# Performance work log

Measured on AMD Instinct MI355X. Metric: run time of the kernel, lower is better.

The kernel has to match this reference:

```python
import jax, jax.numpy as jnp
import numpy as np

N = 50000      # nodes (B*N flattened)
E = 800000     # edges
IN = 128       # in_channels
HID = 32       # hidden_channels per head
HEADS = 2
OUT = 64       # out_channels
NEG_SLOPE = 0.2


def setup_inputs() -> dict:
    key = jax.random.key(0)
    ks = jax.random.split(key, 10)
    x = jax.random.normal(ks[0], (N, IN), jnp.float32)
    edge_index = jax.random.randint(ks[1], (2, E), 0, N, dtype=jnp.int64)
    s = 0.1
    W1 = jax.random.normal(ks[2], (IN, HEADS * HID), jnp.float32) * s
    a_src1 = jax.random.normal(ks[3], (HEADS, HID), jnp.float32) * s
    a_dst1 = jax.random.normal(ks[4], (HEADS, HID), jnp.float32) * s
    b1 = jnp.zeros((HEADS * HID,), jnp.float32)
    W2 = jax.random.normal(ks[5], (HEADS * HID, OUT), jnp.float32) * s
    a_src2 = jax.random.normal(ks[6], (1, OUT), jnp.float32) * s
    a_dst2 = jax.random.normal(ks[7], (1, OUT), jnp.float32) * s
    b2 = jnp.zeros((OUT,), jnp.float32)
    return {"x": x, "edge_index": edge_index,
            "W1": W1, "a_src1": a_src1, "a_dst1": a_dst1, "b1": b1,
            "W2": W2, "a_src2": a_src2, "a_dst2": a_dst2, "b2": b2}


def gat_conv(x, src, dst, W, a_s, a_d, b, heads, ch, concat):
    """PyG GATConv: per-edge attention, softmax over incoming edges of dst."""
    n = x.shape[0]
    h = (x @ W).reshape(n, heads, ch)                       # [N,H,C]
    al_s = (h * a_s).sum(-1)                                # [N,H]
    al_d = (h * a_d).sum(-1)                                # [N,H]
    e = jax.nn.leaky_relu(al_s[src] + al_d[dst], NEG_SLOPE)  # [E,H]
    e_max = jax.ops.segment_max(e, dst, num_segments=n)     # [N,H]
    ex = jnp.exp(e - e_max[dst])
    denom = jax.ops.segment_sum(ex, dst, num_segments=n)
    coef = ex / (denom[dst] + 1e-16)                         # [E,H]
    out = jax.ops.segment_sum(h[src] * coef[:, :, None], dst, num_segments=n)  # [N,H,C]
    out = out.reshape(n, heads * ch) if concat else out.mean(axis=1)
    return out + b


def reference(x, edge_index, W1, a_src1, a_dst1, b1, W2, a_src2, a_dst2, b2):
    loops = jnp.arange(N, dtype=edge_index.dtype)
    src = jnp.concatenate([edge_index[0], loops])  # add_self_loops=True (PyG default)
    dst = jnp.concatenate([edge_index[1], loops])
    h1 = jax.nn.relu(gat_conv(x, src, dst, W1, a_src1, a_dst1, b1, HEADS, HID, True))
    return gat_conv(h1, src, dst, W2, a_src2, a_dst2, b2, 1, OUT, False)
```

## Files before the change

kernel.cpp:

```cpp
#include <hip/hip_runtime.h>

#define IN_CH   128
#define HIDX    64
#define NEG_SLOPE 0.2f
#define CAP     64
#define BNODES  32
#define NXCD    8
#define SUB     4
#define NSEGT   (NXCD * SUB)
#define SEGCAP  64

static inline size_t align256(size_t x) { return (x + 255) & ~(size_t)255; }

__global__ void k_zero(int* __restrict__ p, int n) {
    int i = blockIdx.x * blockDim.x + threadIdx.x;
    if (i < n) p[i] = 0;
}

__global__ void k_bucket(const int* __restrict__ ei, int E,
                         int* __restrict__ bcnt, unsigned* __restrict__ bkt) {
    int i = blockIdx.x * blockDim.x + threadIdx.x;
    if (i >= E) return;
    unsigned xcd;
    asm volatile("s_getreg_b32 %0, hwreg(HW_REG_XCC_ID)" : "=s"(xcd));
    xcd &= (NXCD - 1);
    const int s = ei[i];
    const int d = ei[E + i];
    const int slot = (d >> 5) * NSEGT + (int)xcd * SUB + (i & (SUB - 1));
    int pos = atomicAdd(&bcnt[slot], 1);
    if (pos < SEGCAP)
        bkt[(size_t)slot * SEGCAP + pos] =
            ((unsigned)(d & (BNODES - 1)) << 16) | (unsigned)s;
}

__global__ __launch_bounds__(256)
void k_fill(const int* __restrict__ bcnt, const unsigned* __restrict__ bkt,
            int N, int* __restrict__ cnt, unsigned short* __restrict__ csrf) {
    __shared__ int lcnt[BNODES];
    const int b = blockIdx.x;
    const int t = threadIdx.x;
    if (t < BNODES) lcnt[t] = 0;
    __syncthreads();
    const int nb = b * BNODES;
    const int w = t >> 6, lane = t & 63;
    for (int seg = w; seg < NSEGT; seg += 4) {
        const int slot = b * NSEGT + seg;
        int m = bcnt[slot]; if (m > SEGCAP) m = SEGCAP;
        const unsigned* sp = bkt + (size_t)slot * SEGCAP;
        for (int i = lane; i < m; i += 64) {
            const unsigned v = sp[i];
            const int dl = v >> 16;
            const int s  = v & 0xFFFF;
            const int r  = atomicAdd(&lcnt[dl], 1);
            if (r < CAP) csrf[(size_t)(nb + dl) * CAP + r] = (unsigned short)s;
        }
    }
    __syncthreads();
    if (t < BNODES && nb + t < N) {
        const int c = lcnt[t];
        cnt[nb + t] = c < CAP ? c : CAP;
    }
}

template <int K, int H, bool RELU_IN>
__global__ __launch_bounds__(256)
void k_gemm(const float* __restrict__ X, const float* __restrict__ W,
            const float* __restrict__ bin,
            const float* __restrict__ a_s, const float* __restrict__ a_d,
            float* __restrict__ Hout, float* __restrict__ als,
            float* __restrict__ ald, int N) {
    constexpr int STR = 68;
    __shared__ float Wl[K * 64];
    __shared__ float xT[K * STR];

    const int t  = threadIdx.x;
    const int nb = blockIdx.x * 64;

    {
        const float4* W4 = (const float4*)W;
        float4* Wl4 = (float4*)Wl;
#pragma unroll
        for (int i = 0; i < (K * 16) / 256; ++i)
            Wl4[i * 256 + t] = W4[i * 256 + t];
    }
    {
        constexpr int QK = K / 4;
        constexpr int RS = 256 / QK;
        const int kq = t % QK;
        const int r0 = t / QK;
        for (int n = r0; n < 64; n += RS) {
            const int node = nb + n;
            const int cn = node < N ? node : N - 1;
            float4 v = *(const float4*)(X + (size_t)cn * K + kq * 4);
            if (RELU_IN) {
                const float4 bv = *(const float4*)(bin + kq * 4);
                v.x = fmaxf(v.x + bv.x, 0.f);
                v.y = fmaxf(v.y + bv.y, 0.f);
                v.z = fmaxf(v.z + bv.z, 0.f);
                v.w = fmaxf(v.w + bv.w, 0.f);
            }
            const int ns = (((n >> 2) ^ (kq & 7)) << 2) + (n & 3);
            xT[(kq * 4 + 0) * STR + ns] = v.x;
            xT[(kq * 4 + 1) * STR + ns] = v.y;
            xT[(kq * 4 + 2) * STR + ns] = v.z;
            xT[(kq * 4 + 3) * STR + ns] = v.w;
        }
    }
    __syncthreads();

    const int cg = t & 15;
    const int ng = t >> 4;

    float acc[4][4] = {{0.f}};
#pragma unroll 4
    for (int k = 0; k < K; ++k) {
        const int xb = ((ng ^ ((k >> 2) & 7)) << 2);
        const float4 xv = *(const float4*)&xT[k * STR + xb];
        const float4 wv = *(const float4*)&Wl[k * 64 + (cg << 2)];
        acc[0][0] += xv.x * wv.x; acc[0][1] += xv.x * wv.y;
        acc[0][2] += xv.x * wv.z; acc[0][3] += xv.x * wv.w;
        acc[1][0] += xv.y * wv.x; acc[1][1] += xv.y * wv.y;
        acc[1][2] += xv.y * wv.z; acc[1][3] += xv.y * wv.w;
        acc[2][0] += xv.z * wv.x; acc[2][1] += xv.z * wv.y;
        acc[2][2] += xv.z * wv.z; acc[2][3] += xv.z * wv.w;
        acc[3][0] += xv.w * wv.x; acc[3][1] += xv.w * wv.y;
        acc[3][2] += xv.w * wv.z; acc[3][3] += xv.w * wv.w;
    }

    const float4 asv = *(const float4*)(a_s + cg * 4);
    const float4 adv = *(const float4*)(a_d + cg * 4);
#pragma unroll
    for (int i = 0; i < 4; ++i) {
        const int node = nb + ng * 4 + i;
        float ps = acc[i][0] * asv.x + acc[i][1] * asv.y +
                   acc[i][2] * asv.z + acc[i][3] * asv.w;
        float pd = acc[i][0] * adv.x + acc[i][1] * adv.y +
                   acc[i][2] * adv.z + acc[i][3] * adv.w;
#pragma unroll
        for (int m = 1; m < (H == 2 ? 8 : 16); m <<= 1) {
            ps += __shfl_xor(ps, m, 64);
            pd += __shfl_xor(pd, m, 64);
        }
        if (node < N) {
            *(float4*)(Hout + (size_t)node * 64 + cg * 4) =
                make_float4(acc[i][0], acc[i][1], acc[i][2], acc[i][3]);
            if (H == 2) {
                if ((cg & 7) == 0) {
                    als[node * 2 + (cg >> 3)] = ps;
                    ald[node * 2 + (cg >> 3)] = pd;
                }
            } else if (cg == 0) {
                als[node] = ps;
                ald[node] = pd;
            }
        }
    }
}

template <int H>
__global__ __launch_bounds__(256)
void k_agg(const int* __restrict__ cnt, const unsigned short* __restrict__ csrf,
           const float* __restrict__ als, const float* __restrict__ ald,
           const float* __restrict__ h, const float* __restrict__ bias,
           float* __restrict__ out, int N) {
    int wid = blockIdx.x * 4 + (threadIdx.x >> 6);
    int lane = threadIdx.x & 63;
    if (wid >= N) return;

    const int deg = cnt[wid];
    const int g  = lane >> 4;
    const int cl = lane & 15;
    const int head = (H == 2) ? (cl >> 3) : 0;
    const float aldh = ald[wid * H + head];
    const size_t base = (size_t)wid * CAP;

    float4 acc = make_float4(0.f, 0.f, 0.f, 0.f);
    float dsum = 0.f;

    if (g == 0) {
        float e = als[wid * H + head] + aldh;
        e = e > 0.f ? e : NEG_SLOPE * e;
        const float c = __expf(e);
        dsum = c;
        const float4 hv = *(const float4*)(h + (size_t)wid * 64 + cl * 4);
        acc.x = c * hv.x; acc.y = c * hv.y;
        acc.z = c * hv.z; acc.w = c * hv.w;
    }

#pragma unroll 2
    for (int j = g; j < deg; j += 4) {
        const int s = csrf[base + j];
        float e = als[s * H + head] + aldh;
        e = e > 0.f ? e : NEG_SLOPE * e;
        const float c = __expf(e);
        dsum += c;
        const float4 hv = *(const float4*)(h + (size_t)s * 64 + cl * 4);
        acc.x += c * hv.x; acc.y += c * hv.y;
        acc.z += c * hv.z; acc.w += c * hv.w;
    }
#pragma unroll
    for (int m = 16; m < 64; m <<= 1) {
        acc.x += __shfl_xor(acc.x, m, 64);
        acc.y += __shfl_xor(acc.y, m, 64);
        acc.z += __shfl_xor(acc.z, m, 64);
        acc.w += __shfl_xor(acc.w, m, 64);
        dsum  += __shfl_xor(dsum,  m, 64);
    }
    if (g == 0) {
        const float inv = 1.0f / (dsum + 1e-16f);
        float4 r;
        if (bias) {
            const float4 bv = *(const float4*)(bias + cl * 4);
            r = make_float4(acc.x * inv + bv.x, acc.y * inv + bv.y,
                            acc.z * inv + bv.z, acc.w * inv + bv.w);
        } else {
            r = make_float4(acc.x * inv, acc.y * inv, acc.z * inv, acc.w * inv);
        }
        *(float4*)(out + (size_t)wid * 64 + cl * 4) = r;
    }
}

extern "C" void kernel_launch(void* const* d_in, const int* in_sizes, int n_in,
                              void* d_out, int out_size, void* d_ws, size_t ws_size,
                              hipStream_t stream) {
    const float* x   = (const float*)d_in[0];
    const int*   ei  = (const int*)d_in[1];
    const float* W1  = (const float*)d_in[2];
    const float* as1 = (const float*)d_in[3];
    const float* ad1 = (const float*)d_in[4];
    const float* b1  = (const float*)d_in[5];
    const float* W2  = (const float*)d_in[6];
    const float* as2 = (const float*)d_in[7];
    const float* ad2 = (const float*)d_in[8];
    const float* b2  = (const float*)d_in[9];
    float* out = (float*)d_out;

    const int N    = in_sizes[0] / IN_CH;
    const int E    = in_sizes[1] / 2;
    const int NBUK = (N + BNODES - 1) / BNODES;
    const int NCTR = NBUK * NSEGT;

    char* ws = (char*)d_ws;
    size_t o = 0;
    auto alloc = [&](size_t bytes) { void* p = ws + o; o = align256(o + bytes); return p; };
    int*            cnt  = (int*)alloc((size_t)N * sizeof(int));
    int*            bcnt = (int*)alloc((size_t)NCTR * sizeof(int));
    unsigned*       bkt  = (unsigned*)alloc((size_t)NCTR * SEGCAP * sizeof(unsigned));
    unsigned short* csrf = (unsigned short*)alloc((size_t)N * CAP * sizeof(unsigned short));
    float*          h    = (float*)alloc((size_t)N * 64 * sizeof(float));
    float*          als1 = (float*)alloc((size_t)N * 2 * sizeof(float));
    float*          ald1 = (float*)alloc((size_t)N * 2 * sizeof(float));
    float*          als2 = (float*)alloc((size_t)N * sizeof(float));
    float*          ald2 = (float*)alloc((size_t)N * sizeof(float));
    float*          out1 = out;

    k_zero<<<(NCTR + 255) / 256, 256, 0, stream>>>(bcnt, NCTR);

    k_bucket<<<(E + 255) / 256, 256, 0, stream>>>(ei, E, bcnt, bkt);
    k_fill<<<NBUK, 256, 0, stream>>>(bcnt, bkt, N, cnt, csrf);

    const int gg = (N + 63) / 64;
    const int gn = (N + 3) / 4;

    k_gemm<IN_CH, 2, false><<<gg, 256, 0, stream>>>(x, W1, nullptr, as1, ad1,
                                                    h, als1, ald1, N);
    k_agg<2><<<gn, 256, 0, stream>>>(cnt, csrf, als1, ald1, h, nullptr, out1, N);

    k_gemm<HIDX, 1, true><<<gg, 256, 0, stream>>>(out1, W2, b1, as2, ad2,
                                                  h, als2, ald2, N);
    k_agg<1><<<gn, 256, 0, stream>>>(cnt, csrf, als2, ald2, h, b2, out, N);
}
```

Baseline: 156.5 us.

## Store layer-2 features as bf16 and widen aggregation lanes to 8 channels

```diff
diff --git a/kernel.cpp b/kernel.cpp
--- a/kernel.cpp
+++ b/kernel.cpp
@@ -12,12 +12,19 @@
 
 static inline size_t align256(size_t x) { return (x + 255) & ~(size_t)255; }
 
+__device__ inline unsigned pk_bf16(float a, float b) {
+    unsigned ua = __float_as_uint(a), ub = __float_as_uint(b);
+    ua = (ua + 0x7FFFu + ((ua >> 16) & 1u)) >> 16;
+    ub = (ub + 0x7FFFu + ((ub >> 16) & 1u)) >> 16;
+    return ua | (ub << 16);
+}
+
 __global__ void k_zero(int* __restrict__ p, int n) {
     int i = blockIdx.x * blockDim.x + threadIdx.x;
     if (i < n) p[i] = 0;
 }
 
-__global__ void k_bucket(const int* __restrict__ ei, int E,
+__global__ void k_bucket(const int* __restrict__ ei, int E, int NBUK,
                          int* __restrict__ bcnt, unsigned* __restrict__ bkt) {
     int i = blockIdx.x * blockDim.x + threadIdx.x;
     if (i >= E) return;
@@ -26,7 +33,7 @@
     xcd &= (NXCD - 1);
     const int s = ei[i];
     const int d = ei[E + i];
-    const int slot = (d >> 5) * NSEGT + (int)xcd * SUB + (i & (SUB - 1));
+    const int slot = (int)xcd * (NBUK * SUB) + (d >> 5) * SUB + (i & (SUB - 1));
     int pos = atomicAdd(&bcnt[slot], 1);
     if (pos < SEGCAP)
         bkt[(size_t)slot * SEGCAP + pos] =
@@ -35,7 +42,8 @@
 
 __global__ __launch_bounds__(256)
 void k_fill(const int* __restrict__ bcnt, const unsigned* __restrict__ bkt,
-            int N, int* __restrict__ cnt, unsigned short* __restrict__ csrf) {
+            int N, int NBUK, int* __restrict__ cnt,
+            unsigned short* __restrict__ csrf) {
     __shared__ int lcnt[BNODES];
     const int b = blockIdx.x;
     const int t = threadIdx.x;
@@ -44,7 +52,7 @@
     const int nb = b * BNODES;
     const int w = t >> 6, lane = t & 63;
     for (int seg = w; seg < NSEGT; seg += 4) {
-        const int slot = b * NSEGT + seg;
+        const int slot = (seg >> 2) * (NBUK * SUB) + b * SUB + (seg & 3);
         int m = bcnt[slot]; if (m > SEGCAP) m = SEGCAP;
         const unsigned* sp = bkt + (size_t)slot * SEGCAP;
         for (int i = lane; i < m; i += 64) {
@@ -62,13 +70,13 @@
     }
 }
 
-template <int K, int H, bool RELU_IN>
+template <int K, int H, bool RELU_IN, bool BF16_OUT>
 __global__ __launch_bounds__(256)
 void k_gemm(const float* __restrict__ X, const float* __restrict__ W,
             const float* __restrict__ bin,
             const float* __restrict__ a_s, const float* __restrict__ a_d,
-            float* __restrict__ Hout, float* __restrict__ als,
-            float* __restrict__ ald, int N) {
+            float* __restrict__ HoutF, unsigned short* __restrict__ HoutB,
+            float* __restrict__ als, float* __restrict__ ald, int N) {
     constexpr int STR = 68;
     __shared__ float Wl[K * 64];
     __shared__ float xT[K * STR];
@@ -142,8 +150,15 @@
             pd += __shfl_xor(pd, m, 64);
         }
         if (node < N) {
-            *(float4*)(Hout + (size_t)node * 64 + cg * 4) =
-                make_float4(acc[i][0], acc[i][1], acc[i][2], acc[i][3]);
+            if (BF16_OUT) {
+                uint2 pv;
+                pv.x = pk_bf16(acc[i][0], acc[i][1]);
+                pv.y = pk_bf16(acc[i][2], acc[i][3]);
+                *(uint2*)(HoutB + (size_t)node * 64 + cg * 4) = pv;
+            } else {
+                *(float4*)(HoutF + (size_t)node * 64 + cg * 4) =
+                    make_float4(acc[i][0], acc[i][1], acc[i][2], acc[i][3]);
+            }
             if (H == 2) {
                 if ((cg & 7) == 0) {
                     als[node * 2 + (cg >> 3)] = ps;
@@ -157,66 +172,83 @@
     }
 }
 
-template <int H>
+template <int H, bool BF16H>
 __global__ __launch_bounds__(256)
 void k_agg(const int* __restrict__ cnt, const unsigned short* __restrict__ csrf,
            const float* __restrict__ als, const float* __restrict__ ald,
-           const float* __restrict__ h, const float* __restrict__ bias,
-           float* __restrict__ out, int N) {
+           const float* __restrict__ hF, const unsigned short* __restrict__ hB,
+           const float* __restrict__ bias, float* __restrict__ out, int N) {
     int wid = blockIdx.x * 4 + (threadIdx.x >> 6);
     int lane = threadIdx.x & 63;
     if (wid >= N) return;
 
     const int deg = cnt[wid];
-    const int g  = lane >> 4;
-    const int cl = lane & 15;
-    const int head = (H == 2) ? (cl >> 3) : 0;
+    const int g  = lane >> 3;
+    const int cl = lane & 7;
+    const int head = (H == 2) ? (cl >> 2) : 0;
     const float aldh = ald[wid * H + head];
     const size_t base = (size_t)wid * CAP;
 
-    float4 acc = make_float4(0.f, 0.f, 0.f, 0.f);
+    float4 a0 = make_float4(0.f, 0.f, 0.f, 0.f);
+    float4 a1 = make_float4(0.f, 0.f, 0.f, 0.f);
     float dsum = 0.f;
+
+    auto accum = [&](int s, float c) {
+        if (BF16H) {
+            const uint4 u = *(const uint4*)(hB + (size_t)s * 64 + cl * 8);
+            a0.x += c * __uint_as_float(u.x << 16);
+            a0.y += c * __uint_as_float(u.x & 0xFFFF0000u);
+            a0.z += c * __uint_as_float(u.y << 16);
+            a0.w += c * __uint_as_float(u.y & 0xFFFF0000u);
+            a1.x += c * __uint_as_float(u.z << 16);
+            a1.y += c * __uint_as_float(u.z & 0xFFFF0000u);
+            a1.z += c * __uint_as_float(u.w << 16);
+            a1.w += c * __uint_as_float(u.w & 0xFFFF0000u);
+        } else {
+            const float4* hp = (const float4*)(hF + (size_t)s * 64 + cl * 8);
+            const float4 h0 = hp[0], h1 = hp[1];
+            a0.x += c * h0.x; a0.y += c * h0.y; a0.z += c * h0.z; a0.w += c * h0.w;
+            a1.x += c * h1.x; a1.y += c * h1.y; a1.z += c * h1.z; a1.w += c * h1.w;
+        }
+    };
 
     if (g == 0) {
         float e = als[wid * H + head] + aldh;
         e = e > 0.f ? e : NEG_SLOPE * e;
         const float c = __expf(e);
         dsum = c;
-        const float4 hv = *(const float4*)(h + (size_t)wid * 64 + cl * 4);
-        acc.x = c * hv.x; acc.y = c * hv.y;
-        acc.z = c * hv.z; acc.w = c * hv.w;
+        accum(wid, c);
     }
 
 #pragma unroll 2
-    for (int j = g; j < deg; j += 4) {
+    for (int j = g; j < deg; j += 8) {
         const int s = csrf[base + j];
         float e = als[s * H + head] + aldh;
         e = e > 0.f ? e : NEG_SLOPE * e;
         const float c = __expf(e);
         dsum += c;
-        const float4 hv = *(const float4*)(h + (size_t)s * 64 + cl * 4);
-        acc.x += c * hv.x; acc.y += c * hv.y;
-        acc.z += c * hv.z; acc.w += c * hv.w;
+        accum(s, c);
     }
 #pragma unroll
-    for (int m = 16; m < 64; m <<= 1) {
-        acc.x += __shfl_xor(acc.x, m, 64);
-        acc.y += __shfl_xor(acc.y, m, 64);
-        acc.z += __shfl_xor(acc.z, m, 64);
-        acc.w += __shfl_xor(acc.w, m, 64);
+    for (int m = 8; m < 64; m <<= 1) {
+        a0.x += __shfl_xor(a0.x, m, 64); a0.y += __shfl_xor(a0.y, m, 64);
+        a0.z += __shfl_xor(a0.z, m, 64); a0.w += __shfl_xor(a0.w, m, 64);
+        a1.x += __shfl_xor(a1.x, m, 64); a1.y += __shfl_xor(a1.y, m, 64);
+        a1.z += __shfl_xor(a1.z, m, 64); a1.w += __shfl_xor(a1.w, m, 64);
         dsum  += __shfl_xor(dsum,  m, 64);
     }
     if (g == 0) {
         const float inv = 1.0f / (dsum + 1e-16f);
-        float4 r;
+        a0.x *= inv; a0.y *= inv; a0.z *= inv; a0.w *= inv;
+        a1.x *= inv; a1.y *= inv; a1.z *= inv; a1.w *= inv;
         if (bias) {
-            const float4 bv = *(const float4*)(bias + cl * 4);
-            r = make_float4(acc.x * inv + bv.x, acc.y * inv + bv.y,
-                            acc.z * inv + bv.z, acc.w * inv + bv.w);
-        } else {
-            r = make_float4(acc.x * inv, acc.y * inv, acc.z * inv, acc.w * inv);
-        }
-        *(float4*)(out + (size_t)wid * 64 + cl * 4) = r;
+            const float4* bp = (const float4*)(bias + cl * 8);
+            const float4 b0 = bp[0], b1v = bp[1];
+            a0.x += b0.x;  a0.y += b0.y;  a0.z += b0.z;  a0.w += b0.w;
+            a1.x += b1v.x; a1.y += b1v.y; a1.z += b1v.z; a1.w += b1v.w;
+        }
+        float4* op = (float4*)(out + (size_t)wid * 64 + cl * 8);
+        op[0] = a0; op[1] = a1;
     }
 }
 
@@ -253,20 +285,23 @@
     float*          als2 = (float*)alloc((size_t)N * sizeof(float));
     float*          ald2 = (float*)alloc((size_t)N * sizeof(float));
     float*          out1 = out;
+    unsigned short* h2b  = (unsigned short*)h;
 
     k_zero<<<(NCTR + 255) / 256, 256, 0, stream>>>(bcnt, NCTR);
 
-    k_bucket<<<(E + 255) / 256, 256, 0, stream>>>(ei, E, bcnt, bkt);
-    k_fill<<<NBUK, 256, 0, stream>>>(bcnt, bkt, N, cnt, csrf);
+    k_bucket<<<(E + 255) / 256, 256, 0, stream>>>(ei, E, NBUK, bcnt, bkt);
+    k_fill<<<NBUK, 256, 0, stream>>>(bcnt, bkt, N, NBUK, cnt, csrf);
 
     const int gg = (N + 63) / 64;
     const int gn = (N + 3) / 4;
 
-    k_gemm<IN_CH, 2, false><<<gg, 256, 0, stream>>>(x, W1, nullptr, as1, ad1,
-                                                    h, als1, ald1, N);
-    k_agg<2><<<gn, 256, 0, stream>>>(cnt, csrf, als1, ald1, h, nullptr, out1, N);
-
-    k_gemm<HIDX, 1, true><<<gg, 256, 0, stream>>>(out1, W2, b1, as2, ad2,
-                                                  h, als2, ald2, N);
-    k_agg<1><<<gn, 256, 0, stream>>>(cnt, csrf, als2, ald2, h, b2, out, N);
-}
+    k_gemm<IN_CH, 2, false, false><<<gg, 256, 0, stream>>>(
+        x, W1, nullptr, as1, ad1, h, nullptr, als1, ald1, N);
+    k_agg<2, false><<<gn, 256, 0, stream>>>(
+        cnt, csrf, als1, ald1, h, nullptr, nullptr, out1, N);
+
+    k_gemm<HIDX, 1, true, true><<<gg, 256, 0, stream>>>(
+        out1, W2, b1, as2, ad2, nullptr, h2b, als2, ald2, N);
+    k_agg<1, true><<<gn, 256, 0, stream>>>(
+        cnt, csrf, als2, ald2, nullptr, h2b, b2, out, N);
+}
```

After: 144.1 us. 1.09x faster.
